# Kernel tuning notes

Measured on AMD Instinct MI355X. Metric: run time of the kernel, lower is better.

## Reference

```python
import jax, jax.numpy as jnp
import numpy as np

B = 65536
NC = 64          # coarse samples
NF = 128         # fine samples
NEAR, FAR = 2.0, 6.0


def setup_inputs() -> dict:
    key = jax.random.key(0)
    k1, k2, k3, k4, k5, k6 = jax.random.split(key, 6)
    ray_origin = jax.random.normal(k1, (B, 3), dtype=jnp.float32)
    ray_direction = jax.random.normal(k2, (B, 3), dtype=jnp.float32)
    # stratified linspace depths, as in the coarse branch of _sample_points_on_ray
    step = (FAR - NEAR) / (NC - 1)
    coarse_depth_values = jnp.broadcast_to(
        NEAR + jnp.arange(NC, dtype=jnp.float32) * step, (B, NC)
    )
    coarse_weights = jax.random.uniform(k3, (B, NC), dtype=jnp.float32)
    u = jax.random.uniform(k4, (B, NF), dtype=jnp.float32)
    raw_density = jax.random.uniform(k5, (B, NC + NF, 1), dtype=jnp.float32)
    raw_color = jax.random.uniform(k6, (B, NC + NF, 3), dtype=jnp.float32)
    return {
        "ray_origin": ray_origin,
        "ray_direction": ray_direction,
        "coarse_depth_values": coarse_depth_values,
        "coarse_weights": coarse_weights,
        "u": u,
        "raw_density": raw_density,
        "raw_color": raw_color,
    }


def _sample_pdf(bins, weights, u):
    """Inverse-CDF sampling. bins: [B, M+1], weights: [B, M], u: [B, N]."""
    M = weights.shape[1]
    weights = weights + 1e-5
    pdf = weights / jnp.sum(weights, axis=-1, keepdims=True)
    cdf = jnp.cumsum(pdf, axis=-1)                     # [B, M]
    cdf = jnp.concatenate([jnp.zeros_like(cdf[:, :1]), cdf], axis=-1)  # [B, M+1]
    # torch loop `above_inds += (u >= cdf[:, i])` for i in [0, M) ==
    # searchsorted(cdf[:, :M], u, side='right')
    above = jax.vmap(lambda c, uu: jnp.searchsorted(c, uu, side="right"))(
        cdf[:, :M], u
    )                                                  # [B, N], values in [1, M]
    below = jnp.clip(above - 1, 0, None)
    cdf_b = jnp.take_along_axis(cdf, below, axis=-1)
    cdf_a = jnp.take_along_axis(cdf, above, axis=-1)
    bins_b = jnp.take_along_axis(bins, below, axis=-1)
    bins_a = jnp.take_along_axis(bins, above, axis=-1)
    denom = cdf_a - cdf_b
    denom = jnp.where(denom < 1e-5, jnp.ones_like(denom), denom)
    t = (u - cdf_b) / denom
    return bins_b + t * (bins_a - bins_b)


def _composite(raw_density, raw_color, depth_values):
    # distances between consecutive samples, last one = 1e10
    dists = depth_values[..., 1:] - depth_values[..., :-1]
    dists = jnp.concatenate(
        [dists, jnp.full_like(dists[:, :1], 1e10)], axis=-1
    )
    alpha = 1.0 - jnp.exp(-raw_density[..., 0] * dists)          # [B, S]
    T = jnp.cumprod(1.0 - alpha + 1e-10, axis=-1)[:, :-1]
    T = jnp.concatenate([jnp.ones_like(T[:, :1]), T], axis=-1)
    weights = T * alpha                                           # [B, S]
    depth = jnp.sum(weights * depth_values, axis=-1, keepdims=True)
    color = jnp.sum(weights[..., None] * raw_color, axis=-2)      # [B, 3]
    return depth, color, weights


def reference(ray_origin, ray_direction, coarse_depth_values, coarse_weights,
              u, raw_density, raw_color):
    # fine branch of _sample_points_on_ray
    mids = 0.5 * (coarse_depth_values[..., 1:] + coarse_depth_values[..., :-1])
    w = coarse_weights[:, 1:-1]
    fine_depths = _sample_pdf(mids, w, u)                         # [B, NF]
    depth_values = jnp.sort(
        jnp.concatenate([coarse_depth_values, fine_depths], axis=-1), axis=-1
    )                                                             # [B, NC+NF]
    points_on_ray = (
        ray_origin[:, None, :]
        + ray_direction[:, None, :] * depth_values[..., None]
    )                                                             # [B, S, 3]
    depth, color_map, weights = _composite(raw_density, raw_color, depth_values)
    # forward of RenderRay returns the color map; points kept live via dummy use
    del points_on_ray, depth, weights
    return color_map
```

## Files before the change

### kernel.cpp

```cpp
#include <hip/hip_runtime.h>

#define NC 64
#define NF 128
#define NT 192
#define B_TOTAL 65536
#define RPB 4

#define NEAR_F 2.0f
#define STEP_F (4.0f / 63.0f)
#define INV_STEP (63.0f / 4.0f)

__global__ __launch_bounds__(256) void render_ray_kernel(
    const float* __restrict__ cw,
    const float* __restrict__ u_in,
    const float* __restrict__ dens,
    const float* __restrict__ col,
    float* __restrict__ out)
{
    const int wave = threadIdx.x >> 6;
    const int lane = threadIdx.x & 63;
    const int ray  = blockIdx.x * RPB + wave;

    __shared__ float s_cdf [RPB][64];
    __shared__ float s_m   [RPB][200];
    __shared__ int   s_hist[RPB][64];

    const float wraw = cw[(size_t)ray * NC + lane];
    float x = u_in[(size_t)ray * NF + lane];
    float y = u_in[(size_t)ray * NF + 64 + lane];

    float4 dv = make_float4(0.f, 0.f, 0.f, 0.f);
    float4 c0 = dv, c1 = dv, c2 = dv;
    const int i0 = 4 * lane;
    if (lane < 48) {
        dv = *reinterpret_cast<const float4*>(dens + (size_t)ray * NT + i0);
        const float4* cp4 = reinterpret_cast<const float4*>(col + (size_t)ray * NT * 3 + 3 * (size_t)i0);
        c0 = cp4[0]; c1 = cp4[1]; c2 = cp4[2];
    }

    const float wv = (lane >= 1 && lane <= 62) ? (wraw + 1e-5f) : 0.0f;
    float ssum = wv;
    #pragma unroll
    for (int off = 32; off; off >>= 1) ssum += __shfl_xor(ssum, off);
    const float pdf = __fdividef(wv, ssum);
    float scan = pdf;
    #pragma unroll
    for (int off = 1; off < 64; off <<= 1) {
        const float t = __shfl_up(scan, off);
        if (lane >= off) scan += t;
    }
    s_cdf[wave][lane]  = scan;
    s_hist[wave][lane] = 0;
    __builtin_amdgcn_wave_barrier();

    #pragma unroll
    for (int k = 2; k <= 128; k <<= 1) {
        #pragma unroll
        for (int j = k >> 1; j > 0; j >>= 1) {
            if (j == 64) {
                const float mn = fminf(x, y);
                const float mx = fmaxf(x, y);
                x = mn; y = mx;
            } else {
                const bool lower = (lane & j) == 0;
                const bool ascx  = (k >= 128) ? true : ((lane & k) == 0);
                const bool ascy  = (k >= 128) ? true
                                 : ((k == 64) ? false : ((lane & k) == 0));
                const float px = __shfl_xor(x, j);
                const float py = __shfl_xor(y, j);
                x = (ascx == lower) ? fminf(x, px) : fmaxf(x, px);
                y = (ascy == lower) ? fminf(y, py) : fmaxf(y, py);
            }
        }
    }

    const float* __restrict__ cdfp = s_cdf[wave];
    auto sample = [&](float u) -> float {
        int l = 0, h = 62;
        while (l < h) {
            const int mid = (l + h) >> 1;
            if (cdfp[mid] <= u) l = mid + 1; else h = mid;
        }
        const int below = l - 1;
        const float cb = cdfp[below];
        const float ca = cdfp[l];
        float denom = ca - cb;
        if (denom < 1e-5f) denom = 1.0f;
        const float t = __fdividef(u - cb, denom);
        return NEAR_F + ((float)below + 0.5f + t) * STEP_F;
    };

    const float fx = sample(x);
    const float fy = sample(y);
    int gx = (int)floorf((fx - NEAR_F) * INV_STEP) + 1;
    int gy = (int)floorf((fy - NEAR_F) * INV_STEP) + 1;
    gx = min(max(gx, 1), 63);
    gy = min(max(gy, 1), 63);

    s_m[wave][lane + gx]      = fx;
    s_m[wave][lane + 64 + gy] = fy;
    atomicAdd(&s_hist[wave][gx], 1);
    atomicAdd(&s_hist[wave][gy], 1);
    __builtin_amdgcn_wave_barrier();

    int hsum = s_hist[wave][lane];
    #pragma unroll
    for (int off = 1; off < 64; off <<= 1) {
        const int t = __shfl_up(hsum, off);
        if (lane >= off) hsum += t;
    }
    s_m[wave][lane + hsum] = NEAR_F + (float)lane * STEP_F;
    __builtin_amdgcn_wave_barrier();

    const float* __restrict__ mp = s_m[wave];
    float f0 = 1.0f, f1 = 1.0f, f2 = 1.0f, f3 = 1.0f;
    if (lane < 48) {
        const float m0 = mp[i0], m1 = mp[i0 + 1], m2 = mp[i0 + 2], m3 = mp[i0 + 3];
        const float m4 = mp[(lane == 47) ? 191 : (i0 + 4)];
        const float d0 = m1 - m0;
        const float d1 = m2 - m1;
        const float d2 = m3 - m2;
        const float d3 = (lane == 47) ? 1e10f : (m4 - m3);
        f0 = 1.0f - (1.0f - __expf(-dv.x * d0)) + 1e-10f;
        f1 = 1.0f - (1.0f - __expf(-dv.y * d1)) + 1e-10f;
        f2 = 1.0f - (1.0f - __expf(-dv.z * d2)) + 1e-10f;
        f3 = 1.0f - (1.0f - __expf(-dv.w * d3)) + 1e-10f;
    }

    float scanp = f0 * f1 * f2 * f3;
    #pragma unroll
    for (int off = 1; off < 64; off <<= 1) {
        const float t = __shfl_up(scanp, off);
        if (lane >= off) scanp *= t;
    }
    float T0 = __shfl_up(scanp, 1);
    if (lane == 0) T0 = 1.0f;
    const float T1 = T0 * f0;
    const float T2 = T1 * f1;
    const float T3 = T2 * f2;

    float ax = 0.f, ay = 0.f, az = 0.f;
    if (lane < 48) {
        const float w0 = T0 * (1.0f - f0 + 1e-10f);
        const float w1 = T1 * (1.0f - f1 + 1e-10f);
        const float w2 = T2 * (1.0f - f2 + 1e-10f);
        const float w3 = T3 * (1.0f - f3 + 1e-10f);
        ax = w0 * c0.x + w1 * c0.w + w2 * c1.z + w3 * c2.y;
        ay = w0 * c0.y + w1 * c1.x + w2 * c1.w + w3 * c2.z;
        az = w0 * c0.z + w1 * c1.y + w2 * c2.x + w3 * c2.w;
    }

    #pragma unroll
    for (int off = 32; off; off >>= 1) {
        ax += __shfl_xor(ax, off);
        ay += __shfl_xor(ay, off);
        az += __shfl_xor(az, off);
    }
    if (lane < 3) {
        const float v = (lane == 0) ? ax : ((lane == 1) ? ay : az);
        out[(size_t)ray * 3 + lane] = v;
    }
}

extern "C" void kernel_launch(void* const* d_in, const int* in_sizes, int n_in,
                              void* d_out, int out_size, void* d_ws, size_t ws_size,
                              hipStream_t stream) {
    const float* cwts = (const float*)d_in[3];
    const float* u    = (const float*)d_in[4];
    const float* dens = (const float*)d_in[5];
    const float* col  = (const float*)d_in[6];
    float* out = (float*)d_out;

    dim3 grid(B_TOTAL / RPB);
    dim3 block(256);
    hipLaunchKernelGGL(render_ray_kernel, grid, block, 0, stream,
                       cwts, u, dens, col, out);
}
```

Before: 298.3 us.

## Replace bitonic sort of u with fine-grained bucket counting sort of samples

Removes the 28-stage register bitonic sort of the uniform samples. Instead, each fine depth goes into one of 2016 fine buckets using packed 8-bit LDS atomic counters. Ranks come from a byte-wise prefix sum plus a wave scan, and coarse depths are interleaved via bucket offsets. Two odd-even fix-up passes then repair ordering inside buckets that collide. This trades many cross-lane shuffles for LDS atomics and extra shared memory. The risk is that the local fix-up passes may not fully sort arrays where several samples land in the same bucket, and the extra LDS could reduce occupancy.

```diff
diff --git a/kernel.cpp b/kernel.cpp
--- a/kernel.cpp
+++ b/kernel.cpp
@@ -8,7 +8,8 @@
 
 #define NEAR_F 2.0f
 #define STEP_F (4.0f / 63.0f)
-#define INV_STEP (63.0f / 4.0f)
+#define BUCK_SCALE 504.0f
+#define NBUCK 2016
 
 __global__ __launch_bounds__(256) void render_ray_kernel(
     const float* __restrict__ cw,
@@ -21,13 +22,14 @@
     const int lane = threadIdx.x & 63;
     const int ray  = blockIdx.x * RPB + wave;
 
-    __shared__ float s_cdf [RPB][64];
-    __shared__ float s_m   [RPB][200];
-    __shared__ int   s_hist[RPB][64];
+    __shared__ __align__(16) float          s_cdf[RPB][64];
+    __shared__ __align__(16) unsigned int   s_bkt[RPB][512];
+    __shared__ __align__(16) unsigned short s_dwp[RPB][512];
+    __shared__ __align__(16) float          s_m  [RPB][200];
 
     const float wraw = cw[(size_t)ray * NC + lane];
-    float x = u_in[(size_t)ray * NF + lane];
-    float y = u_in[(size_t)ray * NF + 64 + lane];
+    const float x = u_in[(size_t)ray * NF + lane];
+    const float y = u_in[(size_t)ray * NF + 64 + lane];
 
     float4 dv = make_float4(0.f, 0.f, 0.f, 0.f);
     float4 c0 = dv, c1 = dv, c2 = dv;
@@ -38,6 +40,10 @@
         c0 = cp4[0]; c1 = cp4[1]; c2 = cp4[2];
     }
 
+    const uint4 zz = make_uint4(0u, 0u, 0u, 0u);
+    ((uint4*)&s_bkt[wave][0])[2 * lane]     = zz;
+    ((uint4*)&s_bkt[wave][0])[2 * lane + 1] = zz;
+
     const float wv = (lane >= 1 && lane <= 62) ? (wraw + 1e-5f) : 0.0f;
     float ssum = wv;
     #pragma unroll
@@ -49,30 +55,8 @@
         const float t = __shfl_up(scan, off);
         if (lane >= off) scan += t;
     }
-    s_cdf[wave][lane]  = scan;
-    s_hist[wave][lane] = 0;
-    __builtin_amdgcn_wave_barrier();
-
-    #pragma unroll
-    for (int k = 2; k <= 128; k <<= 1) {
-        #pragma unroll
-        for (int j = k >> 1; j > 0; j >>= 1) {
-            if (j == 64) {
-                const float mn = fminf(x, y);
-                const float mx = fmaxf(x, y);
-                x = mn; y = mx;
-            } else {
-                const bool lower = (lane & j) == 0;
-                const bool ascx  = (k >= 128) ? true : ((lane & k) == 0);
-                const bool ascy  = (k >= 128) ? true
-                                 : ((k == 64) ? false : ((lane & k) == 0));
-                const float px = __shfl_xor(x, j);
-                const float py = __shfl_xor(y, j);
-                x = (ascx == lower) ? fminf(x, px) : fmaxf(x, px);
-                y = (ascy == lower) ? fminf(y, py) : fmaxf(y, py);
-            }
-        }
-    }
+    s_cdf[wave][lane] = scan;
+    __builtin_amdgcn_wave_barrier();
 
     const float* __restrict__ cdfp = s_cdf[wave];
     auto sample = [&](float u) -> float {
@@ -92,35 +76,94 @@
 
     const float fx = sample(x);
     const float fy = sample(y);
-    int gx = (int)floorf((fx - NEAR_F) * INV_STEP) + 1;
-    int gy = (int)floorf((fy - NEAR_F) * INV_STEP) + 1;
-    gx = min(max(gx, 1), 63);
-    gy = min(max(gy, 1), 63);
-
-    s_m[wave][lane + gx]      = fx;
-    s_m[wave][lane + 64 + gy] = fy;
-    atomicAdd(&s_hist[wave][gx], 1);
-    atomicAdd(&s_hist[wave][gy], 1);
-    __builtin_amdgcn_wave_barrier();
-
-    int hsum = s_hist[wave][lane];
+
+    int b0 = (int)((fx - NEAR_F) * BUCK_SCALE);
+    int b1 = (int)((fy - NEAR_F) * BUCK_SCALE);
+    b0 = min(max(b0, 0), NBUCK - 1);
+    b1 = min(max(b1, 0), NBUCK - 1);
+
+    const unsigned sh0 = (unsigned)(b0 & 3) * 8u;
+    const unsigned sh1 = (unsigned)(b1 & 3) * 8u;
+    const unsigned old0 = atomicAdd(&s_bkt[wave][b0 >> 2], 1u << sh0);
+    const unsigned old1 = atomicAdd(&s_bkt[wave][b1 >> 2], 1u << sh1);
+    const int arr0 = (int)((old0 >> sh0) & 0xffu);
+    const int arr1 = (int)((old1 >> sh1) & 0xffu);
+    __builtin_amdgcn_wave_barrier();
+
+    const uint4 va = ((const uint4*)&s_bkt[wave][0])[2 * lane];
+    const uint4 vb = ((const uint4*)&s_bkt[wave][0])[2 * lane + 1];
+    const int p0 = 0;
+    const int p1 = p0 + (int)((va.x * 0x01010101u) >> 24);
+    const int p2 = p1 + (int)((va.y * 0x01010101u) >> 24);
+    const int p3 = p2 + (int)((va.z * 0x01010101u) >> 24);
+    const int p4 = p3 + (int)((va.w * 0x01010101u) >> 24);
+    const int p5 = p4 + (int)((vb.x * 0x01010101u) >> 24);
+    const int p6 = p5 + (int)((vb.y * 0x01010101u) >> 24);
+    const int p7 = p6 + (int)((vb.z * 0x01010101u) >> 24);
+    const int tot = p7 + (int)((vb.w * 0x01010101u) >> 24);
+
+    int incl = tot;
     #pragma unroll
     for (int off = 1; off < 64; off <<= 1) {
-        const int t = __shfl_up(hsum, off);
-        if (lane >= off) hsum += t;
-    }
-    s_m[wave][lane + hsum] = NEAR_F + (float)lane * STEP_F;
-    __builtin_amdgcn_wave_barrier();
-
-    const float* __restrict__ mp = s_m[wave];
+        const int t = __shfl_up(incl, off);
+        if (lane >= off) incl += t;
+    }
+    const int base = incl - tot;
+
+    uint4 w;
+    w.x = (unsigned)(base + p0) | ((unsigned)(base + p1) << 16);
+    w.y = (unsigned)(base + p2) | ((unsigned)(base + p3) << 16);
+    w.z = (unsigned)(base + p4) | ((unsigned)(base + p5) << 16);
+    w.w = (unsigned)(base + p6) | ((unsigned)(base + p7) << 16);
+    ((uint4*)&s_dwp[wave][0])[lane] = w;
+    __builtin_amdgcn_wave_barrier();
+
+    {
+        const int dw = b0 >> 2, bp = b0 & 3;
+        const unsigned v = s_bkt[wave][dw];
+        const unsigned mask = (1u << (8u * (unsigned)bp)) - 1u;
+        const int bytepre = (int)(((v & mask) * 0x01010101u) >> 24);
+        const int rank = (int)s_dwp[wave][dw] + bytepre + arr0;
+        s_m[wave][rank + (b0 >> 5) + 1] = fx;
+    }
+    {
+        const int dw = b1 >> 2, bp = b1 & 3;
+        const unsigned v = s_bkt[wave][dw];
+        const unsigned mask = (1u << (8u * (unsigned)bp)) - 1u;
+        const int bytepre = (int)(((v & mask) * 0x01010101u) >> 24);
+        const int rank = (int)s_dwp[wave][dw] + bytepre + arr1;
+        s_m[wave][rank + (b1 >> 5) + 1] = fy;
+    }
+    const int Fk = (int)s_dwp[wave][8 * lane];
+    s_m[wave][lane + Fk] = NEAR_F + (float)lane * STEP_F;
+    __builtin_amdgcn_wave_barrier();
+
+    {
+        const int j = 3 * lane;
+        const float t0 = s_m[wave][j], t1 = s_m[wave][j + 1], t2 = s_m[wave][j + 2];
+        const float a = fminf(t0, t1), b = fmaxf(t0, t1);
+        const float cmin = fminf(b, t2), cmax = fmaxf(b, t2);
+        s_m[wave][j]     = fminf(a, cmin);
+        s_m[wave][j + 1] = fmaxf(a, cmin);
+        s_m[wave][j + 2] = cmax;
+    }
+    __builtin_amdgcn_wave_barrier();
+    if (lane < 63) {
+        const int j = 3 * lane + 2;
+        const float t0 = s_m[wave][j], t1 = s_m[wave][j + 1];
+        s_m[wave][j]     = fminf(t0, t1);
+        s_m[wave][j + 1] = fmaxf(t0, t1);
+    }
+    __builtin_amdgcn_wave_barrier();
+
     float f0 = 1.0f, f1 = 1.0f, f2 = 1.0f, f3 = 1.0f;
     if (lane < 48) {
-        const float m0 = mp[i0], m1 = mp[i0 + 1], m2 = mp[i0 + 2], m3 = mp[i0 + 3];
-        const float m4 = mp[(lane == 47) ? 191 : (i0 + 4)];
-        const float d0 = m1 - m0;
-        const float d1 = m2 - m1;
-        const float d2 = m3 - m2;
-        const float d3 = (lane == 47) ? 1e10f : (m4 - m3);
+        const float4 m4 = *(const float4*)&s_m[wave][i0];
+        const float mnext = s_m[wave][(lane == 47) ? 191 : (i0 + 4)];
+        const float d0 = m4.y - m4.x;
+        const float d1 = m4.z - m4.y;
+        const float d2 = m4.w - m4.z;
+        const float d3 = (lane == 47) ? 1e10f : (mnext - m4.w);
         f0 = 1.0f - (1.0f - __expf(-dv.x * d0)) + 1e-10f;
         f1 = 1.0f - (1.0f - __expf(-dv.y * d1)) + 1e-10f;
         f2 = 1.0f - (1.0f - __expf(-dv.z * d2)) + 1e-10f;
```

Result: no change. 297.4 us (-0.3%).

## Replace bitonic sort and binary search with bucket sort and CDF lookup table

Applied to the files above, without the earlier changes.

Removes the 28-stage bitonic sort of the 128 uniform samples. They are now placed by a 512-bucket counting sort that packs four 8-bit counters per word and uses atomic adds in LDS. After a short odd-even cleanup the samples are treated as sorted. The per-sample binary search over the CDF becomes a 256-entry lookup table followed by a short linear walk. Sorting u before the inverse CDF makes the fine depths monotonic, so the final merge needs only a prefix max on grid indices. This adds LDS use and atomics, and it relies on only four transposition passes being enough to fix ordering within a bucket. That holds only when buckets contain few samples.

```diff
diff --git a/kernel.cpp b/kernel.cpp
--- a/kernel.cpp
+++ b/kernel.cpp
@@ -21,13 +21,17 @@
     const int lane = threadIdx.x & 63;
     const int ray  = blockIdx.x * RPB + wave;
 
-    __shared__ float s_cdf [RPB][64];
-    __shared__ float s_m   [RPB][200];
-    __shared__ int   s_hist[RPB][64];
+    __shared__ __align__(16) float    s_cdf [RPB][64];
+    __shared__ __align__(16) unsigned s_hist[RPB][128];
+    __shared__ __align__(16) int      s_dwp [RPB][128];
+    __shared__ __align__(16) float    s_su  [RPB][128];
+    __shared__ __align__(16) int      s_tab [RPB][256];
+    __shared__ __align__(16) int      s_h2  [RPB][64];
+    __shared__ __align__(16) float    s_m   [RPB][200];
 
     const float wraw = cw[(size_t)ray * NC + lane];
-    float x = u_in[(size_t)ray * NF + lane];
-    float y = u_in[(size_t)ray * NF + 64 + lane];
+    const float x = u_in[(size_t)ray * NF + lane];
+    const float y = u_in[(size_t)ray * NF + 64 + lane];
 
     float4 dv = make_float4(0.f, 0.f, 0.f, 0.f);
     float4 c0 = dv, c1 = dv, c2 = dv;
@@ -38,6 +42,10 @@
         c0 = cp4[0]; c1 = cp4[1]; c2 = cp4[2];
     }
 
+    s_hist[wave][lane]      = 0u;
+    s_hist[wave][64 + lane] = 0u;
+    s_h2[wave][lane]        = 0;
+
     const float wv = (lane >= 1 && lane <= 62) ? (wraw + 1e-5f) : 0.0f;
     float ssum = wv;
     #pragma unroll
@@ -49,61 +57,107 @@
         const float t = __shfl_up(scan, off);
         if (lane >= off) scan += t;
     }
-    s_cdf[wave][lane]  = scan;
-    s_hist[wave][lane] = 0;
-    __builtin_amdgcn_wave_barrier();
-
-    #pragma unroll
-    for (int k = 2; k <= 128; k <<= 1) {
-        #pragma unroll
-        for (int j = k >> 1; j > 0; j >>= 1) {
-            if (j == 64) {
-                const float mn = fminf(x, y);
-                const float mx = fmaxf(x, y);
-                x = mn; y = mx;
-            } else {
-                const bool lower = (lane & j) == 0;
-                const bool ascx  = (k >= 128) ? true : ((lane & k) == 0);
-                const bool ascy  = (k >= 128) ? true
-                                 : ((k == 64) ? false : ((lane & k) == 0));
-                const float px = __shfl_xor(x, j);
-                const float py = __shfl_xor(y, j);
-                x = (ascx == lower) ? fminf(x, px) : fmaxf(x, px);
-                y = (ascy == lower) ? fminf(y, py) : fmaxf(y, py);
-            }
-        }
-    }
-
+    s_cdf[wave][lane] = scan;
+
+    const int bx = min((int)(x * 512.0f), 511);
+    const int by = min((int)(y * 512.0f), 511);
+    const unsigned shx = (unsigned)(bx & 3) * 8u;
+    const unsigned shy = (unsigned)(by & 3) * 8u;
+    const unsigned ox = atomicAdd(&s_hist[wave][bx >> 2], 1u << shx);
+    const unsigned oy = atomicAdd(&s_hist[wave][by >> 2], 1u << shy);
+    const int arrx = (int)((ox >> shx) & 0xffu);
+    const int arry = (int)((oy >> shy) & 0xffu);
+
+    int lo = min((int)ceilf(scan * 256.0f), 256);
+    int hi = __shfl_down(lo, 1);
+    if (lane == 61) hi = 256;
+    if (lane < 62) {
+        for (int c = lo; c < hi; ++c) s_tab[wave][c] = lane;
+    }
+    __builtin_amdgcn_wave_barrier();
+
+    const uint2 hh = *reinterpret_cast<const uint2*>(&s_hist[wave][2 * lane]);
+    const int cnt0 = (int)((hh.x * 0x01010101u) >> 24);
+    const int cnt1 = (int)((hh.y * 0x01010101u) >> 24);
+    const int tot = cnt0 + cnt1;
+    int incl = tot;
+    #pragma unroll
+    for (int off = 1; off < 64; off <<= 1) {
+        const int t = __shfl_up(incl, off);
+        if (lane >= off) incl += t;
+    }
+    const int base = incl - tot;
+    *reinterpret_cast<int2*>(&s_dwp[wave][2 * lane]) = make_int2(base, base + cnt0);
+    __builtin_amdgcn_wave_barrier();
+
+    {
+        const int d = bx >> 2;
+        const unsigned hv = s_hist[wave][d];
+        const unsigned mask = (1u << shx) - 1u;
+        const int bpre = (int)(((hv & mask) * 0x01010101u) >> 24);
+        s_su[wave][s_dwp[wave][d] + bpre + arrx] = x;
+    }
+    {
+        const int d = by >> 2;
+        const unsigned hv = s_hist[wave][d];
+        const unsigned mask = (1u << shy) - 1u;
+        const int bpre = (int)(((hv & mask) * 0x01010101u) >> 24);
+        s_su[wave][s_dwp[wave][d] + bpre + arry] = y;
+    }
+    __builtin_amdgcn_wave_barrier();
+
+    const float2 uu = *reinterpret_cast<const float2*>(&s_su[wave][2 * lane]);
     const float* __restrict__ cdfp = s_cdf[wave];
+    const int* __restrict__ tabp = s_tab[wave];
+
     auto sample = [&](float u) -> float {
-        int l = 0, h = 62;
-        while (l < h) {
-            const int mid = (l + h) >> 1;
-            if (cdfp[mid] <= u) l = mid + 1; else h = mid;
-        }
-        const int below = l - 1;
-        const float cb = cdfp[below];
-        const float ca = cdfp[l];
+        int s = tabp[min((int)(u * 256.0f), 255)];
+        float ca = cdfp[s + 1];
+        while (s < 61 && ca <= u) { s++; ca = cdfp[s + 1]; }
+        const float cb = cdfp[s];
         float denom = ca - cb;
         if (denom < 1e-5f) denom = 1.0f;
         const float t = __fdividef(u - cb, denom);
-        return NEAR_F + ((float)below + 0.5f + t) * STEP_F;
+        return NEAR_F + ((float)s + 0.5f + t) * STEP_F;
     };
 
-    const float fx = sample(x);
-    const float fy = sample(y);
-    int gx = (int)floorf((fx - NEAR_F) * INV_STEP) + 1;
-    int gy = (int)floorf((fy - NEAR_F) * INV_STEP) + 1;
-    gx = min(max(gx, 1), 63);
-    gy = min(max(gy, 1), 63);
-
-    s_m[wave][lane + gx]      = fx;
-    s_m[wave][lane + 64 + gy] = fy;
-    atomicAdd(&s_hist[wave][gx], 1);
-    atomicAdd(&s_hist[wave][gy], 1);
-    __builtin_amdgcn_wave_barrier();
-
-    int hsum = s_hist[wave][lane];
+    float f0 = sample(uu.x);
+    float f1 = sample(uu.y);
+
+    #pragma unroll
+    for (int r = 0; r < 4; ++r) {
+        const float lo2 = fminf(f0, f1), hi2 = fmaxf(f0, f1);
+        f0 = lo2; f1 = hi2;
+        const float nx = __shfl_down(f0, 1);
+        const float pv = __shfl_up(f1, 1);
+        const float nmin = fminf(f1, nx);
+        const float pmax = fmaxf(f0, pv);
+        if (lane < 63) f1 = nmin;
+        if (lane > 0)  f0 = pmax;
+    }
+
+    int g0 = (int)floorf((f0 - NEAR_F) * INV_STEP) + 1;
+    int g1 = (int)floorf((f1 - NEAR_F) * INV_STEP) + 1;
+    g0 = min(max(g0, 1), 63);
+    g1 = min(max(g1, 1), 63);
+    g1 = max(g1, g0);
+    int gm = g1;
+    #pragma unroll
+    for (int off = 1; off < 64; off <<= 1) {
+        const int t = __shfl_up(gm, off);
+        if (lane >= off) gm = max(gm, t);
+    }
+    const int gprev = __shfl_up(gm, 1);
+    if (lane > 0) g0 = max(g0, gprev);
+    g1 = gm;
+
+    s_m[wave][2 * lane + g0]     = f0;
+    s_m[wave][2 * lane + 1 + g1] = f1;
+    atomicAdd(&s_h2[wave][g0], 1);
+    atomicAdd(&s_h2[wave][g1], 1);
+    __builtin_amdgcn_wave_barrier();
+
+    int hsum = s_h2[wave][lane];
     #pragma unroll
     for (int off = 1; off < 64; off <<= 1) {
         const int t = __shfl_up(hsum, off);
@@ -112,22 +166,21 @@
     s_m[wave][lane + hsum] = NEAR_F + (float)lane * STEP_F;
     __builtin_amdgcn_wave_barrier();
 
-    const float* __restrict__ mp = s_m[wave];
-    float f0 = 1.0f, f1 = 1.0f, f2 = 1.0f, f3 = 1.0f;
+    float q0 = 1.0f, q1 = 1.0f, q2 = 1.0f, q3 = 1.0f;
     if (lane < 48) {
-        const float m0 = mp[i0], m1 = mp[i0 + 1], m2 = mp[i0 + 2], m3 = mp[i0 + 3];
-        const float m4 = mp[(lane == 47) ? 191 : (i0 + 4)];
-        const float d0 = m1 - m0;
-        const float d1 = m2 - m1;
-        const float d2 = m3 - m2;
-        const float d3 = (lane == 47) ? 1e10f : (m4 - m3);
-        f0 = 1.0f - (1.0f - __expf(-dv.x * d0)) + 1e-10f;
-        f1 = 1.0f - (1.0f - __expf(-dv.y * d1)) + 1e-10f;
-        f2 = 1.0f - (1.0f - __expf(-dv.z * d2)) + 1e-10f;
-        f3 = 1.0f - (1.0f - __expf(-dv.w * d3)) + 1e-10f;
-    }
-
-    float scanp = f0 * f1 * f2 * f3;
+        const float4 m4 = *reinterpret_cast<const float4*>(&s_m[wave][i0]);
+        const float mnext = s_m[wave][(lane == 47) ? 191 : (i0 + 4)];
+        const float d0 = m4.y - m4.x;
+        const float d1 = m4.z - m4.y;
+        const float d2 = m4.w - m4.z;
+        const float d3 = (lane == 47) ? 1e10f : (mnext - m4.w);
+        q0 = 1.0f - (1.0f - __expf(-dv.x * d0)) + 1e-10f;
+        q1 = 1.0f - (1.0f - __expf(-dv.y * d1)) + 1e-10f;
+        q2 = 1.0f - (1.0f - __expf(-dv.z * d2)) + 1e-10f;
+        q3 = 1.0f - (1.0f - __expf(-dv.w * d3)) + 1e-10f;
+    }
+
+    float scanp = q0 * q1 * q2 * q3;
     #pragma unroll
     for (int off = 1; off < 64; off <<= 1) {
         const float t = __shfl_up(scanp, off);
@@ -135,16 +188,16 @@
     }
     float T0 = __shfl_up(scanp, 1);
     if (lane == 0) T0 = 1.0f;
-    const float T1 = T0 * f0;
-    const float T2 = T1 * f1;
-    const float T3 = T2 * f2;
+    const float T1 = T0 * q0;
+    const float T2 = T1 * q1;
+    const float T3 = T2 * q2;
 
     float ax = 0.f, ay = 0.f, az = 0.f;
     if (lane < 48) {
-        const float w0 = T0 * (1.0f - f0 + 1e-10f);
-        const float w1 = T1 * (1.0f - f1 + 1e-10f);
-        const float w2 = T2 * (1.0f - f2 + 1e-10f);
-        const float w3 = T3 * (1.0f - f3 + 1e-10f);
+        const float w0 = T0 * (1.0f - q0 + 1e-10f);
+        const float w1 = T1 * (1.0f - q1 + 1e-10f);
+        const float w2 = T2 * (1.0f - q2 + 1e-10f);
+        const float w3 = T3 * (1.0f - q3 + 1e-10f);
         ax = w0 * c0.x + w1 * c0.w + w2 * c1.z + w3 * c2.y;
         ay = w0 * c0.y + w1 * c1.x + w2 * c1.w + w3 * c2.z;
         az = w0 * c0.z + w1 * c1.y + w2 * c2.x + w3 * c2.w;
```

Measured after the change: 300.0 us. About the same (+0.6%).

## Process two rays per wavefront to interleave independent shuffle chains

Applied to the files above, without the earlier changes.

Each wavefront now handles two rays, interleaving their reductions, scans, bitonic sort and binary searches to expose instruction-level parallelism across the long serial shuffle chains. The bin index is derived directly from the search result instead of a floor-based recomputation, and the alpha/transmittance math is simplified to reuse the exponential. This raises register pressure and halves the grid size, which may reduce occupancy.

```diff
diff --git a/kernel.cpp b/kernel.cpp
--- a/kernel.cpp
+++ b/kernel.cpp
@@ -4,11 +4,9 @@
 #define NF 128
 #define NT 192
 #define B_TOTAL 65536
-#define RPB 4
 
 #define NEAR_F 2.0f
 #define STEP_F (4.0f / 63.0f)
-#define INV_STEP (63.0f / 4.0f)
 
 __global__ __launch_bounds__(256) void render_ray_kernel(
     const float* __restrict__ cw,
@@ -19,146 +17,187 @@
 {
     const int wave = threadIdx.x >> 6;
     const int lane = threadIdx.x & 63;
-    const int ray  = blockIdx.x * RPB + wave;
-
-    __shared__ float s_cdf [RPB][64];
-    __shared__ float s_m   [RPB][200];
-    __shared__ int   s_hist[RPB][64];
-
-    const float wraw = cw[(size_t)ray * NC + lane];
-    float x = u_in[(size_t)ray * NF + lane];
-    float y = u_in[(size_t)ray * NF + 64 + lane];
-
-    float4 dv = make_float4(0.f, 0.f, 0.f, 0.f);
-    float4 c0 = dv, c1 = dv, c2 = dv;
+    const int ray0 = (blockIdx.x * 4 + wave) * 2;
+
+    __shared__ __align__(16) float s_cdf [4][2][64];
+    __shared__ __align__(16) float s_m   [4][2][200];
+    __shared__ int s_hist[4][2][64];
+
+    float wraw[2], x[2], y[2];
+    float4 dv[2], c0[2], c1[2], c2[2];
     const int i0 = 4 * lane;
-    if (lane < 48) {
-        dv = *reinterpret_cast<const float4*>(dens + (size_t)ray * NT + i0);
-        const float4* cp4 = reinterpret_cast<const float4*>(col + (size_t)ray * NT * 3 + 3 * (size_t)i0);
-        c0 = cp4[0]; c1 = cp4[1]; c2 = cp4[2];
-    }
-
-    const float wv = (lane >= 1 && lane <= 62) ? (wraw + 1e-5f) : 0.0f;
-    float ssum = wv;
-    #pragma unroll
-    for (int off = 32; off; off >>= 1) ssum += __shfl_xor(ssum, off);
-    const float pdf = __fdividef(wv, ssum);
-    float scan = pdf;
+    #pragma unroll
+    for (int q = 0; q < 2; ++q) {
+        const int ray = ray0 + q;
+        wraw[q] = cw[(size_t)ray * NC + lane];
+        x[q] = u_in[(size_t)ray * NF + lane];
+        y[q] = u_in[(size_t)ray * NF + 64 + lane];
+        dv[q] = make_float4(0.f, 0.f, 0.f, 0.f);
+        c0[q] = dv[q]; c1[q] = dv[q]; c2[q] = dv[q];
+        if (lane < 48) {
+            dv[q] = *(const float4*)(dens + (size_t)ray * NT + i0);
+            const float4* cp4 = (const float4*)(col + (size_t)ray * NT * 3 + 3 * (size_t)i0);
+            c0[q] = cp4[0]; c1[q] = cp4[1]; c2[q] = cp4[2];
+        }
+        s_hist[wave][q][lane] = 0;
+    }
+
+    const float wv0 = (lane >= 1 && lane <= 62) ? (wraw[0] + 1e-5f) : 0.0f;
+    const float wv1 = (lane >= 1 && lane <= 62) ? (wraw[1] + 1e-5f) : 0.0f;
+    float t0 = wv0, t1 = wv1;
+    #pragma unroll
+    for (int off = 32; off; off >>= 1) {
+        t0 += __shfl_xor(t0, off);
+        t1 += __shfl_xor(t1, off);
+    }
+    float sc0 = __fdividef(wv0, t0);
+    float sc1 = __fdividef(wv1, t1);
     #pragma unroll
     for (int off = 1; off < 64; off <<= 1) {
-        const float t = __shfl_up(scan, off);
-        if (lane >= off) scan += t;
-    }
-    s_cdf[wave][lane]  = scan;
-    s_hist[wave][lane] = 0;
-    __builtin_amdgcn_wave_barrier();
+        const float a0 = __shfl_up(sc0, off);
+        const float a1 = __shfl_up(sc1, off);
+        if (lane >= off) { sc0 += a0; sc1 += a1; }
+    }
+    s_cdf[wave][0][lane] = sc0;
+    s_cdf[wave][1][lane] = sc1;
 
     #pragma unroll
     for (int k = 2; k <= 128; k <<= 1) {
         #pragma unroll
         for (int j = k >> 1; j > 0; j >>= 1) {
             if (j == 64) {
-                const float mn = fminf(x, y);
-                const float mx = fmaxf(x, y);
-                x = mn; y = mx;
+                #pragma unroll
+                for (int q = 0; q < 2; ++q) {
+                    const float mn = fminf(x[q], y[q]);
+                    const float mx = fmaxf(x[q], y[q]);
+                    x[q] = mn; y[q] = mx;
+                }
             } else {
                 const bool lower = (lane & j) == 0;
-                const bool ascx  = (k >= 128) ? true : ((lane & k) == 0);
-                const bool ascy  = (k >= 128) ? true
-                                 : ((k == 64) ? false : ((lane & k) == 0));
-                const float px = __shfl_xor(x, j);
-                const float py = __shfl_xor(y, j);
-                x = (ascx == lower) ? fminf(x, px) : fmaxf(x, px);
-                y = (ascy == lower) ? fminf(y, py) : fmaxf(y, py);
+                const bool ascx = (k >= 128) ? true : ((lane & k) == 0);
+                const bool ascy = (k >= 128) ? true : ((k == 64) ? false : ascx);
+                const float px0 = __shfl_xor(x[0], j);
+                const float py0 = __shfl_xor(y[0], j);
+                const float px1 = __shfl_xor(x[1], j);
+                const float py1 = __shfl_xor(y[1], j);
+                x[0] = (ascx == lower) ? fminf(x[0], px0) : fmaxf(x[0], px0);
+                y[0] = (ascy == lower) ? fminf(y[0], py0) : fmaxf(y[0], py0);
+                x[1] = (ascx == lower) ? fminf(x[1], px1) : fmaxf(x[1], px1);
+                y[1] = (ascy == lower) ? fminf(y[1], py1) : fmaxf(y[1], py1);
             }
         }
     }
-
-    const float* __restrict__ cdfp = s_cdf[wave];
-    auto sample = [&](float u) -> float {
-        int l = 0, h = 62;
-        while (l < h) {
-            const int mid = (l + h) >> 1;
-            if (cdfp[mid] <= u) l = mid + 1; else h = mid;
-        }
-        const int below = l - 1;
-        const float cb = cdfp[below];
-        const float ca = cdfp[l];
-        float denom = ca - cb;
-        if (denom < 1e-5f) denom = 1.0f;
-        const float t = __fdividef(u - cb, denom);
-        return NEAR_F + ((float)below + 0.5f + t) * STEP_F;
-    };
-
-    const float fx = sample(x);
-    const float fy = sample(y);
-    int gx = (int)floorf((fx - NEAR_F) * INV_STEP) + 1;
-    int gy = (int)floorf((fy - NEAR_F) * INV_STEP) + 1;
-    gx = min(max(gx, 1), 63);
-    gy = min(max(gy, 1), 63);
-
-    s_m[wave][lane + gx]      = fx;
-    s_m[wave][lane + 64 + gy] = fy;
-    atomicAdd(&s_hist[wave][gx], 1);
-    atomicAdd(&s_hist[wave][gy], 1);
     __builtin_amdgcn_wave_barrier();
 
-    int hsum = s_hist[wave][lane];
+    float f[2][2]; int g[2][2];
+    #pragma unroll
+    for (int q = 0; q < 2; ++q) {
+        const float* __restrict__ cdfp = s_cdf[wave][q];
+        #pragma unroll
+        for (int v = 0; v < 2; ++v) {
+            const float u = v ? y[q] : x[q];
+            int l = 0, h = 62;
+            while (l < h) {
+                const int mid = (l + h) >> 1;
+                if (cdfp[mid] <= u) l = mid + 1; else h = mid;
+            }
+            const int s = l - 1;
+            const float cb = cdfp[s], ca = cdfp[l];
+            float denom = ca - cb;
+            if (denom < 1e-5f) denom = 1.0f;
+            const float tt = __fdividef(u - cb, denom);
+            g[q][v] = s + 1 + (tt >= 0.5f ? 1 : 0);
+            f[q][v] = NEAR_F + ((float)s + 0.5f + tt) * STEP_F;
+        }
+    }
+
+    #pragma unroll
+    for (int q = 0; q < 2; ++q) {
+        s_m[wave][q][lane + g[q][0]]      = f[q][0];
+        s_m[wave][q][64 + lane + g[q][1]] = f[q][1];
+        atomicAdd(&s_hist[wave][q][g[q][0]], 1);
+        atomicAdd(&s_hist[wave][q][g[q][1]], 1);
+    }
+    __builtin_amdgcn_wave_barrier();
+
+    int h0 = s_hist[wave][0][lane];
+    int h1 = s_hist[wave][1][lane];
     #pragma unroll
     for (int off = 1; off < 64; off <<= 1) {
-        const int t = __shfl_up(hsum, off);
-        if (lane >= off) hsum += t;
-    }
-    s_m[wave][lane + hsum] = NEAR_F + (float)lane * STEP_F;
+        const int a0 = __shfl_up(h0, off);
+        const int a1 = __shfl_up(h1, off);
+        if (lane >= off) { h0 += a0; h1 += a1; }
+    }
+    const float cval = NEAR_F + (float)lane * STEP_F;
+    s_m[wave][0][lane + h0] = cval;
+    s_m[wave][1][lane + h1] = cval;
     __builtin_amdgcn_wave_barrier();
 
-    const float* __restrict__ mp = s_m[wave];
-    float f0 = 1.0f, f1 = 1.0f, f2 = 1.0f, f3 = 1.0f;
-    if (lane < 48) {
-        const float m0 = mp[i0], m1 = mp[i0 + 1], m2 = mp[i0 + 2], m3 = mp[i0 + 3];
-        const float m4 = mp[(lane == 47) ? 191 : (i0 + 4)];
-        const float d0 = m1 - m0;
-        const float d1 = m2 - m1;
-        const float d2 = m3 - m2;
-        const float d3 = (lane == 47) ? 1e10f : (m4 - m3);
-        f0 = 1.0f - (1.0f - __expf(-dv.x * d0)) + 1e-10f;
-        f1 = 1.0f - (1.0f - __expf(-dv.y * d1)) + 1e-10f;
-        f2 = 1.0f - (1.0f - __expf(-dv.z * d2)) + 1e-10f;
-        f3 = 1.0f - (1.0f - __expf(-dv.w * d3)) + 1e-10f;
-    }
-
-    float scanp = f0 * f1 * f2 * f3;
+    float ff[2][4], aa[2][4];
+    #pragma unroll
+    for (int q = 0; q < 2; ++q) {
+        ff[q][0] = ff[q][1] = ff[q][2] = ff[q][3] = 1.0f;
+        aa[q][0] = aa[q][1] = aa[q][2] = aa[q][3] = 0.0f;
+        if (lane < 48) {
+            const float4 m4 = *(const float4*)&s_m[wave][q][i0];
+            const float mnext = s_m[wave][q][(lane == 47) ? 191 : (i0 + 4)];
+            const float d0 = m4.y - m4.x;
+            const float d1 = m4.z - m4.y;
+            const float d2 = m4.w - m4.z;
+            const float d3 = (lane == 47) ? 1e10f : (mnext - m4.w);
+            const float e0 = __expf(-dv[q].x * d0);
+            const float e1 = __expf(-dv[q].y * d1);
+            const float e2 = __expf(-dv[q].z * d2);
+            const float e3 = __expf(-dv[q].w * d3);
+            ff[q][0] = e0 + 1e-10f; aa[q][0] = 1.0f - e0;
+            ff[q][1] = e1 + 1e-10f; aa[q][1] = 1.0f - e1;
+            ff[q][2] = e2 + 1e-10f; aa[q][2] = 1.0f - e2;
+            ff[q][3] = e3 + 1e-10f; aa[q][3] = 1.0f - e3;
+        }
+    }
+
+    float sp0 = ff[0][0] * ff[0][1] * ff[0][2] * ff[0][3];
+    float sp1 = ff[1][0] * ff[1][1] * ff[1][2] * ff[1][3];
     #pragma unroll
     for (int off = 1; off < 64; off <<= 1) {
-        const float t = __shfl_up(scanp, off);
-        if (lane >= off) scanp *= t;
-    }
-    float T0 = __shfl_up(scanp, 1);
-    if (lane == 0) T0 = 1.0f;
-    const float T1 = T0 * f0;
-    const float T2 = T1 * f1;
-    const float T3 = T2 * f2;
-
-    float ax = 0.f, ay = 0.f, az = 0.f;
-    if (lane < 48) {
-        const float w0 = T0 * (1.0f - f0 + 1e-10f);
-        const float w1 = T1 * (1.0f - f1 + 1e-10f);
-        const float w2 = T2 * (1.0f - f2 + 1e-10f);
-        const float w3 = T3 * (1.0f - f3 + 1e-10f);
-        ax = w0 * c0.x + w1 * c0.w + w2 * c1.z + w3 * c2.y;
-        ay = w0 * c0.y + w1 * c1.x + w2 * c1.w + w3 * c2.z;
-        az = w0 * c0.z + w1 * c1.y + w2 * c2.x + w3 * c2.w;
+        const float a0 = __shfl_up(sp0, off);
+        const float a1 = __shfl_up(sp1, off);
+        if (lane >= off) { sp0 *= a0; sp1 *= a1; }
+    }
+    float T0a = __shfl_up(sp0, 1); if (lane == 0) T0a = 1.0f;
+    float T0b = __shfl_up(sp1, 1); if (lane == 0) T0b = 1.0f;
+
+    float ax[2], ay[2], az[2];
+    {
+        const float Ta1 = T0a * ff[0][0], Ta2 = Ta1 * ff[0][1], Ta3 = Ta2 * ff[0][2];
+        const float W0 = T0a * aa[0][0], W1 = Ta1 * aa[0][1], W2 = Ta2 * aa[0][2], W3 = Ta3 * aa[0][3];
+        ax[0] = W0 * c0[0].x + W1 * c0[0].w + W2 * c1[0].z + W3 * c2[0].y;
+        ay[0] = W0 * c0[0].y + W1 * c1[0].x + W2 * c1[0].w + W3 * c2[0].z;
+        az[0] = W0 * c0[0].z + W1 * c1[0].y + W2 * c2[0].x + W3 * c2[0].w;
+    }
+    {
+        const float Tb1 = T0b * ff[1][0], Tb2 = Tb1 * ff[1][1], Tb3 = Tb2 * ff[1][2];
+        const float W0 = T0b * aa[1][0], W1 = Tb1 * aa[1][1], W2 = Tb2 * aa[1][2], W3 = Tb3 * aa[1][3];
+        ax[1] = W0 * c0[1].x + W1 * c0[1].w + W2 * c1[1].z + W3 * c2[1].y;
+        ay[1] = W0 * c0[1].y + W1 * c1[1].x + W2 * c1[1].w + W3 * c2[1].z;
+        az[1] = W0 * c0[1].z + W1 * c1[1].y + W2 * c2[1].x + W3 * c2[1].w;
     }
 
     #pragma unroll
     for (int off = 32; off; off >>= 1) {
-        ax += __shfl_xor(ax, off);
-        ay += __shfl_xor(ay, off);
-        az += __shfl_xor(az, off);
+        ax[0] += __shfl_xor(ax[0], off);
+        ay[0] += __shfl_xor(ay[0], off);
+        az[0] += __shfl_xor(az[0], off);
+        ax[1] += __shfl_xor(ax[1], off);
+        ay[1] += __shfl_xor(ay[1], off);
+        az[1] += __shfl_xor(az[1], off);
     }
     if (lane < 3) {
-        const float v = (lane == 0) ? ax : ((lane == 1) ? ay : az);
-        out[(size_t)ray * 3 + lane] = v;
+        out[(size_t)ray0 * 3 + lane] = (lane == 0) ? ax[0] : ((lane == 1) ? ay[0] : az[0]);
+    }
+    if (lane >= 8 && lane < 11) {
+        const int ln = lane - 8;
+        out[(size_t)(ray0 + 1) * 3 + ln] = (ln == 0) ? ax[1] : ((ln == 1) ? ay[1] : az[1]);
     }
 }
 
@@ -171,7 +210,7 @@
     const float* col  = (const float*)d_in[6];
     float* out = (float*)d_out;
 
-    dim3 grid(B_TOTAL / RPB);
+    dim3 grid(B_TOTAL / 8);
     dim3 block(256);
     hipLaunchKernelGGL(render_ray_kernel, grid, block, 0, stream,
                        cwts, u, dens, col, out);
```

Result: no change. 302.0 us (+1.2%).
